# Optimization experiments

Measured on AMD Instinct MI355X. Metric: run time of the kernel, lower is better.

Reference implementation:

```python
import jax, jax.numpy as jnp
import numpy as np

H, N, SEQ = 256, 64, 4096

def setup_inputs() -> dict:
    key = jax.random.key(0)
    kA, kB, kC, kdt = jax.random.split(key, 4)
    W = jax.random.normal(kA, (H, N, N), dtype=jnp.float32)
    # Hurwitz (stable) A: skew-symmetric part minus 0.5*I, like HiPPO-style stable transitions
    A = 0.5 * (W - jnp.swapaxes(W, -1, -2)) - 0.5 * jnp.eye(N, dtype=jnp.float32)
    B = jax.random.normal(kB, (H, N), dtype=jnp.float32)
    C = jax.random.normal(kC, (H, N), dtype=jnp.float32)
    # log_dt around log(0.01), matching typical S4 timescale init
    log_dt = jax.random.normal(kdt, (H,), dtype=jnp.float32) * 0.5 + jnp.log(0.01)
    return {"A": A, "B": B, "C": C, "log_dt": log_dt, "L": SEQ}

def _bilinear(dt, A, B):
    # dt: (H,), A: (H,N,N), B: (H,N)
    n = A.shape[-1]
    I = jnp.eye(n, dtype=A.dtype)
    A_back = I - (dt[:, None, None] / 2) * A   # (H,N,N)
    A_fwd = I + (dt[:, None, None] / 2) * A    # (H,N,N)
    dA = jnp.linalg.solve(A_back, A_fwd)                       # (H,N,N)
    dB = dt[:, None] * jnp.linalg.solve(A_back, B[..., None])[..., 0]  # (H,N)
    return dA, dB

def _krylov(L, dA, dB, C):
    # K[h, l] = C[h] @ dA[h]^l @ dB[h], computed by squaring/doubling
    x = dB[..., None]  # (H, N, 1)
    A_ = dA
    while x.shape[-1] < L:
        x2 = jnp.einsum('hmn,hnl->hml', A_, x)  # apply current power
        x = jnp.concatenate([x, x2], axis=-1)
        if x.shape[-1] < L:
            A_ = jnp.einsum('hmn,hnk->hmk', A_, A_)  # square the power
    x = x[..., :L]  # (H, N, L)
    return jnp.einsum('hn,hnl->hl', C, x)  # (H, L)

def reference(A, B, C, log_dt, L):
    dt = jnp.exp(log_dt)
    dA, dB = _bilinear(dt, A, B)
    return _krylov(L, dA, dB, C)
```

## Files before the change

kernel.cpp:

```cpp
#include <hip/hip_runtime.h>

constexpr int STRU = 68;

typedef short v8s __attribute__((ext_vector_type(8)));
typedef float v4f __attribute__((ext_vector_type(4)));

__device__ __forceinline__ unsigned packhl(float x) {
    unsigned xb = __builtin_bit_cast(unsigned, x);
    unsigned hb = xb & 0xffff0000u;
    float lof = x - __builtin_bit_cast(float, hb);
    unsigned lb = __builtin_bit_cast(unsigned, lof) + 0x8000u;
    return __builtin_amdgcn_perm(xb, lb, 0x07060302u);
}

__device__ __forceinline__ float unpackf(unsigned v) {
    float h = __builtin_bit_cast(float, v & 0xffff0000u);
    float l = __builtin_bit_cast(float, v << 16);
    return h + l;
}

__device__ __forceinline__ void load_frag(const unsigned* p, v8s& hi, v8s& lo) {
    uint4 a = *(const uint4*)p;
    uint4 b = *(const uint4*)(p + 4);
    uint4 hw, lw;
    hw.x = __builtin_amdgcn_perm(a.y, a.x, 0x07060302u);
    hw.y = __builtin_amdgcn_perm(a.w, a.z, 0x07060302u);
    hw.z = __builtin_amdgcn_perm(b.y, b.x, 0x07060302u);
    hw.w = __builtin_amdgcn_perm(b.w, b.z, 0x07060302u);
    lw.x = __builtin_amdgcn_perm(a.y, a.x, 0x05040100u);
    lw.y = __builtin_amdgcn_perm(a.w, a.z, 0x05040100u);
    lw.z = __builtin_amdgcn_perm(b.y, b.x, 0x05040100u);
    lw.w = __builtin_amdgcn_perm(b.w, b.z, 0x05040100u);
    hi = __builtin_bit_cast(v8s, hw);
    lo = __builtin_bit_cast(v8s, lw);
}

#define MFMA __builtin_amdgcn_mfma_f32_16x16x32_bf16

template<int MODE>
__device__ __forceinline__ void mm64(const unsigned* __restrict__ P,
                                     const unsigned* __restrict__ Q,
                                     unsigned* D, unsigned* DT, float* G,
                                     const unsigned* R, float ca, float cb,
                                     int tid) {
    const int lane = tid & 63, w = tid >> 6;
    const int nh = lane & 15, qh = lane >> 4;
    const int tr = w >> 1, tc0 = (w & 1) << 1;
    v4f acc[2] = {v4f{0,0,0,0}, v4f{0,0,0,0}};
    #pragma unroll
    for (int kk = 0; kk < 2; ++kk) {
        const int kc = kk * 32 + qh * 8;
        v8s ph, pl, q0h, q0l, q1h, q1l;
        load_frag(P + (tr * 16 + nh) * STRU + kc, ph, pl);
        load_frag(Q + (tc0 * 16 + nh) * STRU + kc, q0h, q0l);
        load_frag(Q + ((tc0 + 1) * 16 + nh) * STRU + kc, q1h, q1l);
        acc[0] = MFMA(ph, q0h, acc[0], 0, 0, 0);
        acc[0] = MFMA(ph, q0l, acc[0], 0, 0, 0);
        acc[0] = MFMA(pl, q0h, acc[0], 0, 0, 0);
        acc[1] = MFMA(ph, q1h, acc[1], 0, 0, 0);
        acc[1] = MFMA(ph, q1l, acc[1], 0, 0, 0);
        acc[1] = MFMA(pl, q1h, acc[1], 0, 0, 0);
    }
    const int row0 = tr * 16 + qh * 4;
    #pragma unroll
    for (int c = 0; c < 2; ++c) {
        const int col = (tc0 + c) * 16 + nh;
        if constexpr (MODE == 2) {
            #pragma unroll
            for (int e = 0; e < 4; ++e) G[(row0 + e) * 64 + col] = acc[c][e];
        } else if constexpr (MODE == 0) {
            #pragma unroll
            for (int e = 0; e < 4; ++e)
                D[(row0 + e) * STRU + col] = packhl(acc[c][e]);
        } else if constexpr (MODE == 1) {
            #pragma unroll
            for (int e = 0; e < 4; ++e) {
                float v = acc[c][e] + ((row0 + e) == col ? 1.0f : 0.0f);
                D[(row0 + e) * STRU + col] = packhl(v);
            }
        } else if constexpr (MODE == 3) {
            uint4 tp;
            #pragma unroll
            for (int e = 0; e < 4; ++e) {
                unsigned pk = packhl(acc[c][e]);
                D[(row0 + e) * STRU + col] = pk;
                ((unsigned*)&tp)[e] = pk;
            }
            *(uint4*)&DT[col * STRU + row0] = tp;
        } else if constexpr (MODE == 4) {
            #pragma unroll
            for (int e = 0; e < 4; ++e) {
                float dv = ca * acc[c][e];
                float dg = ((row0 + e) == col) ? 1.0f : 0.0f;
                D[(row0 + e) * STRU + col]  = packhl(dv);
                DT[(row0 + e) * STRU + col] = packhl(dv + dg);
            }
        } else if constexpr (MODE == 5) {
            #pragma unroll
            for (int e = 0; e < 4; ++e) {
                float t  = unpackf(R[(row0 + e) * STRU + col]);
                float dg = ((row0 + e) == col) ? 1.0f : 0.0f;
                float base = ca * t - dg;
                float sv   = cb * acc[c][e];
                D[(row0 + e) * STRU + col]  = packhl(base + sv);
                DT[(row0 + e) * STRU + col] = packhl(base - sv);
            }
        }
    }
}

__device__ __forceinline__ void dbl64(unsigned* Xt, const unsigned* M, int k, int tid) {
    const int lane = tid & 63, w = tid >> 6;
    const int nh = lane & 15, qh = lane >> 4;
    const int nt = (k + 15) >> 4;
    if (w < 4 * nt) {
        const int t = w >> 2, cb = w & 3;
        v4f acc = {0, 0, 0, 0};
        #pragma unroll
        for (int kk = 0; kk < 2; ++kk) {
            const int kc = kk * 32 + qh * 8;
            v8s ph, pl, mh, ml;
            load_frag(Xt + (t * 16 + nh) * STRU + kc, ph, pl);
            load_frag(M + (cb * 16 + nh) * STRU + kc, mh, ml);
            acc = MFMA(ph, mh, acc, 0, 0, 0);
            acc = MFMA(ph, ml, acc, 0, 0, 0);
            acc = MFMA(pl, mh, acc, 0, 0, 0);
        }
        #pragma unroll
        for (int e = 0; e < 4; ++e) {
            const int j = t * 16 + qh * 4 + e;
            if (j < k) Xt[(k + j) * STRU + cb * 16 + nh] = packhl(acc[e]);
        }
    }
}

__launch_bounds__(512)
__global__ void krylov_kernel(const float* __restrict__ A,
                              const float* __restrict__ Bv,
                              const float* __restrict__ Cv,
                              const float* __restrict__ logdt,
                              float* __restrict__ out)
{
    const int h    = blockIdx.x;
    const int tid  = threadIdx.x;
    const int lane = tid & 63;
    const int w    = tid >> 6;

    __shared__ __align__(16) unsigned SM[6][64 * STRU];
    __shared__ float Bl[64];

    const float dt = expf(logdt[h]);
    const float c  = 0.5f * dt;
    const float al = 1.0f + 0.5f * c;
    const float sd = -(c * c) / (al * al);
    const float c1 = 2.0f / al;
    const float c2 = 2.0f * c / (al * al);

    const float* Ah = A + (size_t)h * 4096;

    for (int idx = tid; idx < 1024; idx += 512) {
        const int r = idx >> 4, c0 = (idx & 15) * 4;
        float4 v = *(const float4*)(Ah + idx * 4);
        if (r == c0 + 0) v.x += 0.5f;
        if (r == c0 + 1) v.y += 0.5f;
        if (r == c0 + 2) v.z += 0.5f;
        if (r == c0 + 3) v.w += 0.5f;
        uint4 pk = make_uint4(packhl(v.x), packhl(v.y), packhl(v.z), packhl(v.w));
        *(uint4*)&SM[0][r * STRU + c0] = pk;
    }
    if (tid < 64) Bl[tid] = Bv[h * 64 + tid];
    else if (tid < 128) SM[5][tid - 64] = packhl(Cv[h * 64 + (tid - 64)]);
    __syncthreads();

    mm64<4>(SM[0], SM[0], SM[1], SM[2], nullptr, nullptr, sd, 0.f, tid);
    __syncthreads();
    mm64<1>(SM[1], SM[2], SM[3], nullptr, nullptr, nullptr, 0.f, 0.f, tid);
    __syncthreads();
    mm64<1>(SM[1], SM[3], SM[2], nullptr, nullptr, nullptr, 0.f, 0.f, tid);
    __syncthreads();
    mm64<1>(SM[1], SM[2], SM[3], nullptr, nullptr, nullptr, 0.f, 0.f, tid);
    __syncthreads();
    mm64<5>(SM[0], SM[3], SM[2], SM[1], nullptr, SM[3], c1, c2, tid);
    __syncthreads();

    if (w == 0) {
        const unsigned* Xr = SM[2] + lane * STRU;
        float acc = 0.0f;
        #pragma unroll
        for (int m4 = 0; m4 < 16; ++m4) {
            uint4 xv = *(const uint4*)(Xr + 4 * m4);
            float4 b4 = *(const float4*)&Bl[4 * m4];
            acc += unpackf(xv.x) * b4.x + unpackf(xv.y) * b4.y
                 + unpackf(xv.z) * b4.z + unpackf(xv.w) * b4.w;
        }
        SM[4][lane] = packhl(c * (acc + Bl[lane]));
    }
    __syncthreads();

    unsigned *bX = SM[2], *bXT = SM[1], *bN = SM[0], *bNT = SM[3];
    #pragma unroll 1
    for (int s = 0; s < 6; ++s) {
        mm64<3>(bX, bXT, bN, bNT, nullptr, nullptr, 0.f, 0.f, tid);
        dbl64(SM[4], bX, 1 << s, tid);
        __syncthreads();
        unsigned* t0 = bX;  bX  = bN;  bN  = t0;
        t0 = bXT; bXT = bNT; bNT = t0;
    }

    #pragma unroll 1
    for (int s = 0; s < 6; ++s) {
        if (s < 5) mm64<3>(bX, bXT, bN, bNT, nullptr, nullptr, 0.f, 0.f, tid);
        dbl64(SM[5], bXT, 1 << s, tid);
        __syncthreads();
        if (s < 5) {
            unsigned* t0 = bX;  bX  = bN;  bN  = t0;
            t0 = bXT; bXT = bNT; bNT = t0;
        }
    }

    mm64<2>(SM[5], SM[4], nullptr, nullptr, out + (size_t)h * 4096, nullptr,
            0.f, 0.f, tid);
}

extern "C" void kernel_launch(void* const* d_in, const int* in_sizes, int n_in,
                              void* d_out, int out_size, void* d_ws, size_t ws_size,
                              hipStream_t stream) {
    const float* A  = (const float*)d_in[0];
    const float* B  = (const float*)d_in[1];
    const float* C  = (const float*)d_in[2];
    const float* ld = (const float*)d_in[3];
    float* out = (float*)d_out;
    const int H = in_sizes[3];
    krylov_kernel<<<H, 512, 0, stream>>>(A, B, C, ld, out);
}
```

Baseline: 79.63 us.

## Switch to 32x32 MFMA tiles and restructure Neumann-series inverse for parallel powers

Replaces the 16x16x32 MFMA path with 32x32x16 bf16 MFMA tiles, where each of four waves computes one 32x32 output tile using split accumulators. The series-based inverse now computes S, S^2, S^3 and S^4 with the last two in parallel, then sums them once instead of running three dependent Horner-style multiplies. dB is built from two matrix-vector passes instead of an extra matrix product. The doubling steps run their Krylov extension on separate waves alongside the power squaring. Only four to six of the eight waves do MFMA work in each phase, and the changed series evaluation may alter numerical accuracy.

```diff
diff --git a/kernel.cpp b/kernel.cpp
--- a/kernel.cpp
+++ b/kernel.cpp
@@ -2,8 +2,8 @@
 
 constexpr int STRU = 68;
 
-typedef short v8s __attribute__((ext_vector_type(8)));
-typedef float v4f __attribute__((ext_vector_type(4)));
+typedef short v8s  __attribute__((ext_vector_type(8)));
+typedef float v16f __attribute__((ext_vector_type(16)));
 
 __device__ __forceinline__ unsigned packhl(float x) {
     unsigned xb = __builtin_bit_cast(unsigned, x);
@@ -35,102 +35,54 @@
     lo = __builtin_bit_cast(v8s, lw);
 }
 
-#define MFMA __builtin_amdgcn_mfma_f32_16x16x32_bf16
-
-template<int MODE>
-__device__ __forceinline__ void mm64(const unsigned* __restrict__ P,
-                                     const unsigned* __restrict__ Q,
-                                     unsigned* D, unsigned* DT, float* G,
-                                     const unsigned* R, float ca, float cb,
-                                     int tid) {
-    const int lane = tid & 63, w = tid >> 6;
-    const int nh = lane & 15, qh = lane >> 4;
-    const int tr = w >> 1, tc0 = (w & 1) << 1;
-    v4f acc[2] = {v4f{0,0,0,0}, v4f{0,0,0,0}};
-    #pragma unroll
-    for (int kk = 0; kk < 2; ++kk) {
-        const int kc = kk * 32 + qh * 8;
-        v8s ph, pl, q0h, q0l, q1h, q1l;
-        load_frag(P + (tr * 16 + nh) * STRU + kc, ph, pl);
-        load_frag(Q + (tc0 * 16 + nh) * STRU + kc, q0h, q0l);
-        load_frag(Q + ((tc0 + 1) * 16 + nh) * STRU + kc, q1h, q1l);
-        acc[0] = MFMA(ph, q0h, acc[0], 0, 0, 0);
-        acc[0] = MFMA(ph, q0l, acc[0], 0, 0, 0);
-        acc[0] = MFMA(pl, q0h, acc[0], 0, 0, 0);
-        acc[1] = MFMA(ph, q1h, acc[1], 0, 0, 0);
-        acc[1] = MFMA(ph, q1l, acc[1], 0, 0, 0);
-        acc[1] = MFMA(pl, q1h, acc[1], 0, 0, 0);
-    }
-    const int row0 = tr * 16 + qh * 4;
-    #pragma unroll
-    for (int c = 0; c < 2; ++c) {
-        const int col = (tc0 + c) * 16 + nh;
-        if constexpr (MODE == 2) {
-            #pragma unroll
-            for (int e = 0; e < 4; ++e) G[(row0 + e) * 64 + col] = acc[c][e];
-        } else if constexpr (MODE == 0) {
-            #pragma unroll
-            for (int e = 0; e < 4; ++e)
-                D[(row0 + e) * STRU + col] = packhl(acc[c][e]);
-        } else if constexpr (MODE == 1) {
-            #pragma unroll
-            for (int e = 0; e < 4; ++e) {
-                float v = acc[c][e] + ((row0 + e) == col ? 1.0f : 0.0f);
-                D[(row0 + e) * STRU + col] = packhl(v);
-            }
-        } else if constexpr (MODE == 3) {
-            uint4 tp;
-            #pragma unroll
-            for (int e = 0; e < 4; ++e) {
-                unsigned pk = packhl(acc[c][e]);
-                D[(row0 + e) * STRU + col] = pk;
-                ((unsigned*)&tp)[e] = pk;
-            }
-            *(uint4*)&DT[col * STRU + row0] = tp;
-        } else if constexpr (MODE == 4) {
-            #pragma unroll
-            for (int e = 0; e < 4; ++e) {
-                float dv = ca * acc[c][e];
-                float dg = ((row0 + e) == col) ? 1.0f : 0.0f;
-                D[(row0 + e) * STRU + col]  = packhl(dv);
-                DT[(row0 + e) * STRU + col] = packhl(dv + dg);
-            }
-        } else if constexpr (MODE == 5) {
-            #pragma unroll
-            for (int e = 0; e < 4; ++e) {
-                float t  = unpackf(R[(row0 + e) * STRU + col]);
-                float dg = ((row0 + e) == col) ? 1.0f : 0.0f;
-                float base = ca * t - dg;
-                float sv   = cb * acc[c][e];
-                D[(row0 + e) * STRU + col]  = packhl(base + sv);
-                DT[(row0 + e) * STRU + col] = packhl(base - sv);
-            }
-        }
-    }
-}
-
-__device__ __forceinline__ void dbl64(unsigned* Xt, const unsigned* M, int k, int tid) {
-    const int lane = tid & 63, w = tid >> 6;
-    const int nh = lane & 15, qh = lane >> 4;
-    const int nt = (k + 15) >> 4;
-    if (w < 4 * nt) {
-        const int t = w >> 2, cb = w & 3;
-        v4f acc = {0, 0, 0, 0};
-        #pragma unroll
-        for (int kk = 0; kk < 2; ++kk) {
-            const int kc = kk * 32 + qh * 8;
-            v8s ph, pl, mh, ml;
-            load_frag(Xt + (t * 16 + nh) * STRU + kc, ph, pl);
-            load_frag(M + (cb * 16 + nh) * STRU + kc, mh, ml);
-            acc = MFMA(ph, mh, acc, 0, 0, 0);
-            acc = MFMA(ph, ml, acc, 0, 0, 0);
-            acc = MFMA(pl, mh, acc, 0, 0, 0);
-        }
+#define MFMA32 __builtin_amdgcn_mfma_f32_32x32x16_bf16
+
+__device__ __forceinline__ v16f tile32(const unsigned* __restrict__ P,
+                                       const unsigned* __restrict__ Q,
+                                       int tr, int tc, int lane) {
+    const int r = lane & 31, hh = lane >> 5;
+    v16f a0, a1;
+    #pragma unroll
+    for (int i = 0; i < 16; ++i) { a0[i] = 0.0f; a1[i] = 0.0f; }
+    #pragma unroll
+    for (int kk = 0; kk < 4; ++kk) {
+        const int kc = kk * 16 + hh * 8;
+        v8s ph, pl, qh, ql;
+        load_frag(P + (tr * 32 + r) * STRU + kc, ph, pl);
+        load_frag(Q + (tc * 32 + r) * STRU + kc, qh, ql);
+        a0 = MFMA32(ph, qh, a0, 0, 0, 0);
+        a1 = MFMA32(ph, ql, a1, 0, 0, 0);
+        a1 = MFMA32(pl, qh, a1, 0, 0, 0);
+    }
+    return a0 + a1;
+}
+
+__device__ __forceinline__ void store_pk(unsigned* D, int tr, int tc, int lane,
+                                         const v16f& a, float sc) {
+    const int r = lane & 31, hh = lane >> 5;
+    #pragma unroll
+    for (int g = 0; g < 4; ++g)
         #pragma unroll
         for (int e = 0; e < 4; ++e) {
-            const int j = t * 16 + qh * 4 + e;
-            if (j < k) Xt[(k + j) * STRU + cb * 16 + nh] = packhl(acc[e]);
-        }
+            const int row = tr * 32 + 8 * g + 4 * hh + e;
+            D[row * STRU + tc * 32 + r] = packhl(sc * a[4 * g + e]);
+        }
+}
+
+__device__ __forceinline__ void store_dual(unsigned* D, unsigned* DT, int tr, int tc,
+                                           int lane, const v16f& a) {
+    const int r = lane & 31, hh = lane >> 5;
+    #pragma unroll
+    for (int g = 0; g < 4; ++g) {
+        uint4 tp;
+        #pragma unroll
+        for (int e = 0; e < 4; ++e) {
+            const int row = tr * 32 + 8 * g + 4 * hh + e;
+            unsigned pk = packhl(a[4 * g + e]);
+            D[row * STRU + tc * 32 + r] = pk;
+            ((unsigned*)&tp)[e] = pk;
+        }
+        *(uint4*)&DT[(tc * 32 + r) * STRU + tr * 32 + 8 * g + 4 * hh] = tp;
     }
 }
 
@@ -145,9 +97,10 @@
     const int tid  = threadIdx.x;
     const int lane = tid & 63;
     const int w    = tid >> 6;
+    const int r    = lane & 31, hh = lane >> 5;
 
     __shared__ __align__(16) unsigned SM[6][64 * STRU];
-    __shared__ float Bl[64];
+    __shared__ float Bl[64], tmv[64];
 
     const float dt = expf(logdt[h]);
     const float c  = 0.5f * dt;
@@ -155,53 +108,120 @@
     const float sd = -(c * c) / (al * al);
     const float c1 = 2.0f / al;
     const float c2 = 2.0f * c / (al * al);
+    const float k1 = dt / al;
+    const float k2 = dt * c / (al * al);
 
     const float* Ah = A + (size_t)h * 4096;
 
     for (int idx = tid; idx < 1024; idx += 512) {
-        const int r = idx >> 4, c0 = (idx & 15) * 4;
+        const int rr = idx >> 4, c0 = (idx & 15) * 4;
         float4 v = *(const float4*)(Ah + idx * 4);
-        if (r == c0 + 0) v.x += 0.5f;
-        if (r == c0 + 1) v.y += 0.5f;
-        if (r == c0 + 2) v.z += 0.5f;
-        if (r == c0 + 3) v.w += 0.5f;
+        if (rr == c0 + 0) v.x += 0.5f;
+        if (rr == c0 + 1) v.y += 0.5f;
+        if (rr == c0 + 2) v.z += 0.5f;
+        if (rr == c0 + 3) v.w += 0.5f;
         uint4 pk = make_uint4(packhl(v.x), packhl(v.y), packhl(v.z), packhl(v.w));
-        *(uint4*)&SM[0][r * STRU + c0] = pk;
+        *(uint4*)&SM[0][rr * STRU + c0] = pk;
     }
     if (tid < 64) Bl[tid] = Bv[h * 64 + tid];
     else if (tid < 128) SM[5][tid - 64] = packhl(Cv[h * 64 + (tid - 64)]);
     __syncthreads();
 
-    mm64<4>(SM[0], SM[0], SM[1], SM[2], nullptr, nullptr, sd, 0.f, tid);
-    __syncthreads();
-    mm64<1>(SM[1], SM[2], SM[3], nullptr, nullptr, nullptr, 0.f, 0.f, tid);
-    __syncthreads();
-    mm64<1>(SM[1], SM[3], SM[2], nullptr, nullptr, nullptr, 0.f, 0.f, tid);
-    __syncthreads();
-    mm64<1>(SM[1], SM[2], SM[3], nullptr, nullptr, nullptr, 0.f, 0.f, tid);
-    __syncthreads();
-    mm64<5>(SM[0], SM[3], SM[2], SM[1], nullptr, SM[3], c1, c2, tid);
-    __syncthreads();
-
-    if (w == 0) {
-        const unsigned* Xr = SM[2] + lane * STRU;
-        float acc = 0.0f;
+    if (w < 4) {
+        v16f a = tile32(SM[0], SM[0], w >> 1, w & 1, lane);
+        store_pk(SM[1], w >> 1, w & 1, lane, a, sd);
+    }
+    __syncthreads();
+    if (w < 4) {
+        v16f a = tile32(SM[1], SM[1], w >> 1, w & 1, lane);
+        store_pk(SM[2], w >> 1, w & 1, lane, a, 1.0f);
+    }
+    __syncthreads();
+    if (w < 4) {
+        v16f a = tile32(SM[1], SM[2], w >> 1, w & 1, lane);
+        store_pk(SM[3], w >> 1, w & 1, lane, a, 1.0f);
+    } else {
+        const int u = w - 4;
+        v16f a = tile32(SM[2], SM[2], u >> 1, u & 1, lane);
+        store_pk(SM[4], u >> 1, u & 1, lane, a, 1.0f);
+    }
+    __syncthreads();
+    for (int idx = tid; idx < 1024; idx += 512) {
+        const int rr = idx >> 4, c0 = (idx & 15) * 4;
+        const int ad = rr * STRU + c0;
+        uint4 x1 = *(const uint4*)&SM[1][ad];
+        uint4 x2 = *(const uint4*)&SM[2][ad];
+        uint4 x3 = *(const uint4*)&SM[3][ad];
+        uint4 x4 = *(const uint4*)&SM[4][ad];
+        float t0 = unpackf(x1.x) + unpackf(x2.x) + unpackf(x3.x) + unpackf(x4.x)
+                 + (rr == c0 + 0 ? 1.0f : 0.0f);
+        float t1 = unpackf(x1.y) + unpackf(x2.y) + unpackf(x3.y) + unpackf(x4.y)
+                 + (rr == c0 + 1 ? 1.0f : 0.0f);
+        float t2 = unpackf(x1.z) + unpackf(x2.z) + unpackf(x3.z) + unpackf(x4.z)
+                 + (rr == c0 + 2 ? 1.0f : 0.0f);
+        float t3 = unpackf(x1.w) + unpackf(x2.w) + unpackf(x3.w) + unpackf(x4.w)
+                 + (rr == c0 + 3 ? 1.0f : 0.0f);
+        uint4 pk = make_uint4(packhl(t0), packhl(t1), packhl(t2), packhl(t3));
+        *(uint4*)&SM[1][ad] = pk;
+    }
+    __syncthreads();
+    if (w < 4) {
+        const int tr = w >> 1, tc = w & 1;
+        v16f a = tile32(SM[0], SM[1], tr, tc, lane);
+        #pragma unroll
+        for (int g = 0; g < 4; ++g)
+            #pragma unroll
+            for (int e = 0; e < 4; ++e) {
+                const int row = tr * 32 + 8 * g + 4 * hh + e;
+                const int col = tc * 32 + r;
+                float t  = unpackf(SM[1][row * STRU + col]);
+                float dg = (row == col) ? 1.0f : 0.0f;
+                float base = c1 * t - dg;
+                float sv   = c2 * a[4 * g + e];
+                SM[2][row * STRU + col] = packhl(base + sv);
+                SM[3][row * STRU + col] = packhl(base - sv);
+            }
+    } else if (w == 4) {
+        float acc1 = 0.0f;
         #pragma unroll
         for (int m4 = 0; m4 < 16; ++m4) {
-            uint4 xv = *(const uint4*)(Xr + 4 * m4);
+            uint4 tv = *(const uint4*)&SM[1][lane * STRU + 4 * m4];
             float4 b4 = *(const float4*)&Bl[4 * m4];
-            acc += unpackf(xv.x) * b4.x + unpackf(xv.y) * b4.y
-                 + unpackf(xv.z) * b4.z + unpackf(xv.w) * b4.w;
-        }
-        SM[4][lane] = packhl(c * (acc + Bl[lane]));
-    }
-    __syncthreads();
-
-    unsigned *bX = SM[2], *bXT = SM[1], *bN = SM[0], *bNT = SM[3];
+            acc1 += unpackf(tv.x) * b4.x + unpackf(tv.y) * b4.y
+                  + unpackf(tv.z) * b4.z + unpackf(tv.w) * b4.w;
+        }
+        tmv[lane] = acc1;
+        __threadfence_block();
+        float acc2 = 0.0f;
+        #pragma unroll
+        for (int m4 = 0; m4 < 16; ++m4) {
+            uint4 sv = *(const uint4*)&SM[0][lane * STRU + 4 * m4];
+            float4 t4 = *(const float4*)&tmv[4 * m4];
+            acc2 += unpackf(sv.x) * t4.x + unpackf(sv.y) * t4.y
+                  + unpackf(sv.z) * t4.z + unpackf(sv.w) * t4.w;
+        }
+        SM[4][lane] = packhl(k1 * acc1 + k2 * acc2);
+    }
+    __syncthreads();
+
+    unsigned *bX = SM[2], *bXT = SM[3], *bN = SM[0], *bNT = SM[1];
     #pragma unroll 1
     for (int s = 0; s < 6; ++s) {
-        mm64<3>(bX, bXT, bN, bNT, nullptr, nullptr, 0.f, 0.f, tid);
-        dbl64(SM[4], bX, 1 << s, tid);
+        if (w < 4) {
+            v16f a = tile32(bX, bXT, w >> 1, w & 1, lane);
+            store_dual(bN, bNT, w >> 1, w & 1, lane, a);
+        } else if (w < 6) {
+            const int k = 1 << s;
+            v16f a = tile32(SM[4], bX, 0, w - 4, lane);
+            #pragma unroll
+            for (int g = 0; g < 4; ++g)
+                #pragma unroll
+                for (int e = 0; e < 4; ++e) {
+                    const int j = 8 * g + 4 * hh + e;
+                    if (j < k)
+                        SM[4][(k + j) * STRU + (w - 4) * 32 + r] = packhl(a[4 * g + e]);
+                }
+        }
         __syncthreads();
         unsigned* t0 = bX;  bX  = bN;  bN  = t0;
         t0 = bXT; bXT = bNT; bNT = t0;
@@ -209,8 +229,21 @@
 
     #pragma unroll 1
     for (int s = 0; s < 6; ++s) {
-        if (s < 5) mm64<3>(bX, bXT, bN, bNT, nullptr, nullptr, 0.f, 0.f, tid);
-        dbl64(SM[5], bXT, 1 << s, tid);
+        if (w < 4 && s < 5) {
+            v16f a = tile32(bX, bXT, w >> 1, w & 1, lane);
+            store_dual(bN, bNT, w >> 1, w & 1, lane, a);
+        } else if (w >= 4 && w < 6) {
+            const int k = 1 << s;
+            v16f a = tile32(SM[5], bXT, 0, w - 4, lane);
+            #pragma unroll
+            for (int g = 0; g < 4; ++g)
+                #pragma unroll
+                for (int e = 0; e < 4; ++e) {
+                    const int j = 8 * g + 4 * hh + e;
+                    if (j < k)
+                        SM[5][(k + j) * STRU + (w - 4) * 32 + r] = packhl(a[4 * g + e]);
+                }
+        }
         __syncthreads();
         if (s < 5) {
             unsigned* t0 = bX;  bX  = bN;  bN  = t0;
@@ -218,8 +251,18 @@
         }
     }
 
-    mm64<2>(SM[5], SM[4], nullptr, nullptr, out + (size_t)h * 4096, nullptr,
-            0.f, 0.f, tid);
+    if (w < 4) {
+        const int tr = w >> 1, tc = w & 1;
+        v16f a = tile32(SM[5], SM[4], tr, tc, lane);
+        float* oh = out + (size_t)h * 4096;
+        #pragma unroll
+        for (int g = 0; g < 4; ++g)
+            #pragma unroll
+            for (int e = 0; e < 4; ++e) {
+                const int row = tr * 32 + 8 * g + 4 * hh + e;
+                oh[row * 64 + tc * 32 + r] = a[4 * g + e];
+            }
+    }
 }
 
 extern "C" void kernel_launch(void* const* d_in, const int* in_sizes, int n_in,
```

New measurement: 81.36 us. 1.02x slower.
